# Optimization experiments

Measured on AMD Instinct MI355X. Metric: run time of the kernel, lower is better.

## Reference

```python
import jax, jax.numpy as jnp
import numpy as np

NH, NKV, HD = 16, 4, 128
ROPE_THETA = 10000.0


def setup_inputs() -> dict:
    key = jax.random.key(0)
    ks = jax.random.split(key, 5)
    std = jnp.float32(0.02)
    return {
        "hidden_states": jax.random.normal(ks[0], (1, 2048, 2048), jnp.float32),
        "wq": jax.random.normal(ks[1], (2048, NH * HD), jnp.float32) * std,
        "wk": jax.random.normal(ks[2], (2048, NKV * HD), jnp.float32) * std,
        "wv": jax.random.normal(ks[3], (2048, NKV * HD), jnp.float32) * std,
        "wo": jax.random.normal(ks[4], (NH * HD, 2048), jnp.float32) * std,
    }


def _rope(x, cos, sin):
    # x: [B,S,n,hd]; pairs (even,odd) treated as complex, multiplied by cis(angle)
    xr = x.reshape(*x.shape[:-1], HD // 2, 2)
    re, im = xr[..., 0], xr[..., 1]
    c = cos[None, :, None, :]  # [1,S,1,hd/2]
    s = sin[None, :, None, :]
    out = jnp.stack((re * c - im * s, re * s + im * c), axis=-1)
    return out.reshape(x.shape)


def reference(hidden_states, wq, wk, wv, wo):
    B, S, H = hidden_states.shape
    q = (hidden_states @ wq).reshape(B, S, NH, HD)
    k = (hidden_states @ wk).reshape(B, S, NKV, HD)
    v = (hidden_states @ wv).reshape(B, S, NKV, HD)

    # precompute_freqs_cis (full rotary dim, rot_dim=None)
    freqs = 1.0 / (ROPE_THETA ** (jnp.arange(0, HD, 2, dtype=jnp.float32) / HD))
    ang = jnp.outer(jnp.arange(S, dtype=jnp.float32), freqs)  # [S, hd/2]
    cos, sin = jnp.cos(ang), jnp.sin(ang)

    q = _rope(q.astype(jnp.float32), cos, sin)
    k = _rope(k.astype(jnp.float32), cos, sin)

    # GQA: repeat_kv == repeat_interleave over head axis
    n_rep = NH // NKV
    k = jnp.repeat(k, n_rep, axis=2)  # [B,S,NH,HD]
    v = jnp.repeat(v, n_rep, axis=2)

    scale = jnp.float32(1.0 / np.sqrt(HD))
    scores = jnp.einsum("bqhd,bkhd->bhqk", q, k) * scale
    causal = jnp.tril(jnp.ones((S, S), dtype=bool))
    scores = jnp.where(causal[None, None], scores, jnp.float32(-1e9))
    attn = jax.nn.softmax(scores, axis=-1)
    out = jnp.einsum("bhqk,bkhd->bqhd", attn, v).reshape(B, S, NH * HD)
    return out @ wo
```

## Files before the change

### kernel.cpp

```cpp
#include <hip/hip_runtime.h>
#include <cstdint>

typedef __attribute__((ext_vector_type(8))) short short8;
typedef __attribute__((ext_vector_type(4))) float f32x4;

static __device__ __forceinline__ unsigned short f2bf(float x) {
  union { float f; unsigned int u; } c; c.f = x;
  unsigned int u = c.u;
  unsigned int r = (u + 0x7fffu + ((u >> 16) & 1u)) >> 16;
  return (unsigned short)r;
}

static __device__ __forceinline__ float bf2f(unsigned short x) {
  union { unsigned int u; float f; } c; c.u = ((unsigned int)x) << 16;
  return c.f;
}

static __device__ __forceinline__ void gl_lds16(const void* g, void* l) {
  __builtin_amdgcn_global_load_lds((const __attribute__((address_space(1))) void*)g,
                                   (__attribute__((address_space(3))) void*)l, 16, 0, 0);
}

__global__ __launch_bounds__(256) void k_sincos(float2* __restrict__ ctab) {
  int idx = blockIdx.x * 256 + threadIdx.x;
  int s = idx >> 6, i = idx & 63;
  float freq = powf(10000.0f, -(float)i / 64.0f);
  float sn, cs;
  sincosf((float)s * freq, &sn, &cs);
  ctab[idx] = make_float2(cs, sn);
}

__global__ __launch_bounds__(256) void k_f32_to_bf16(const float* __restrict__ src,
                                                     unsigned short* __restrict__ dst,
                                                     int n4) {
  int i = blockIdx.x * 256 + threadIdx.x;
  if (i >= n4) return;
  float4 v = reinterpret_cast<const float4*>(src)[i];
  ushort4 o;
  o.x = f2bf(v.x); o.y = f2bf(v.y); o.z = f2bf(v.z); o.w = f2bf(v.w);
  reinterpret_cast<ushort4*>(dst)[i] = o;
}

__global__ __launch_bounds__(256) void k_transpose_all(const float* __restrict__ wq,
                                                       const float* __restrict__ wk,
                                                       const float* __restrict__ wv,
                                                       const float* __restrict__ wo,
                                                       unsigned short* __restrict__ wqt,
                                                       unsigned short* __restrict__ wkt,
                                                       unsigned short* __restrict__ wvt,
                                                       unsigned short* __restrict__ wot) {
  __shared__ float tile[32][33];
  int id = blockIdx.x;
  const float* src; unsigned short* dst; int N, t;
  if (id < 4096)       { src = wq; dst = wqt; N = 2048; t = id; }
  else if (id < 8192)  { src = wo; dst = wot; N = 2048; t = id - 4096; }
  else if (id < 9216)  { src = wk; dst = wkt; N = 512;  t = id - 8192; }
  else                 { src = wv; dst = wvt; N = 512;  t = id - 9216; }
  const int K = 2048;
  int ntx = N >> 5;
  int bn = (t % ntx) * 32, bk = (t / ntx) * 32;
  int tx = threadIdx.x & 31, ty = threadIdx.x >> 5;
#pragma unroll
  for (int i = 0; i < 32; i += 8)
    tile[ty + i][tx] = src[(size_t)(bk + ty + i) * N + bn + tx];
  __syncthreads();
#pragma unroll
  for (int i = 0; i < 32; i += 8)
    dst[(size_t)(bn + ty + i) * K + bk + tx] = f2bf(tile[tx][ty + i]);
}

__global__ __launch_bounds__(256) void k_gemm_bf16(const unsigned short* __restrict__ A,
                                                   const unsigned short* __restrict__ Bt,
                                                   float* __restrict__ C,
                                                   unsigned short* __restrict__ Qd,
                                                   unsigned short* __restrict__ Kd,
                                                   unsigned short* __restrict__ VT,
                                                   const float2* __restrict__ ctab,
                                                   int M, int N, int K, int fuse) {
  __shared__ short sA[2][128 * 64];
  __shared__ short sB[2][64 * 64];
  int tid = threadIdx.x;
  int lane = tid & 63, wid = tid >> 6;
  int wr = wid >> 1, wc = wid & 1;

  int gx = gridDim.x, nwg = gx * gridDim.y;
  int flat = blockIdx.y * gx + blockIdx.x;
  int l = (flat & 7) * (nwg >> 3) + (flat >> 3);
  int bx = l % gx, by = l / gx;
  int m0 = by * 128, n0 = bx * 64;

  f32x4 acc[4][2] = {};

  int srcCol = (((tid & 7) ^ ((tid >> 3) & 7)) << 3);
  int rA = tid >> 3;
  const unsigned short* Ag = A + (size_t)(m0 + rA) * K + srcCol;
  const unsigned short* Bg = Bt + (size_t)(n0 + rA) * K + srcCol;
  int wb = (tid & ~63) * 8;

  int g = lane >> 4, fr = lane & 15, sw = fr & 7;

#define STAGE_G(buf, kof) do { \
    gl_lds16(Ag + (kof),                    &sA[buf][wb]); \
    gl_lds16(Ag + 32 * (size_t)K + (kof),   &sA[buf][2048 + wb]); \
    gl_lds16(Ag + 64 * (size_t)K + (kof),   &sA[buf][4096 + wb]); \
    gl_lds16(Ag + 96 * (size_t)K + (kof),   &sA[buf][6144 + wb]); \
    gl_lds16(Bg + (kof),                    &sB[buf][wb]); \
    gl_lds16(Bg + 32 * (size_t)K + (kof),   &sB[buf][2048 + wb]); \
  } while (0)

  int nt = K >> 6;
  STAGE_G(0, 0);
  __syncthreads();

  int cur = 0;
  for (int t = 0; t < nt; t++) {
    if (t + 1 < nt) STAGE_G(cur ^ 1, (size_t)((t + 1) << 6));
    const short* sAc = sA[cur];
    const short* sBc = sB[cur];
#pragma unroll
    for (int kk = 0; kk < 2; kk++) {
      int so = ((((kk << 2) + g) ^ sw) << 3);
      short8 af[4], bf2[2];
#pragma unroll
      for (int x = 0; x < 4; x++)
        af[x] = *(const short8*)(sAc + (wr * 64 + x * 16 + fr) * 64 + so);
#pragma unroll
      for (int ni = 0; ni < 2; ni++)
        bf2[ni] = *(const short8*)(sBc + (wc * 32 + ni * 16 + fr) * 64 + so);
#pragma unroll
      for (int x = 0; x < 4; x++)
#pragma unroll
        for (int ni = 0; ni < 2; ni++)
          acc[x][ni] = __builtin_amdgcn_mfma_f32_16x16x32_bf16(af[x], bf2[ni], acc[x][ni], 0, 0, 0);
    }
    __syncthreads();
    cur ^= 1;
  }
#undef STAGE_G

  int rb = m0 + wr * 64 + (g << 2);
  if (!fuse) {
#pragma unroll
    for (int ni = 0; ni < 2; ni++) {
      int col = n0 + wc * 32 + ni * 16 + fr;
#pragma unroll
      for (int x = 0; x < 4; x++)
#pragma unroll
        for (int j = 0; j < 4; j++)
          C[(size_t)(rb + x * 16 + j) * N + col] = acc[x][ni][j];
    }
    return;
  }

  const float QAMP = 0.12751742836257666f;
#pragma unroll
  for (int ni = 0; ni < 2; ni++) {
    int col = n0 + wc * 32 + ni * 16 + fr;
    if (col >= 2560) {
#pragma unroll
      for (int x = 0; x < 4; x++) {
        ushort4 pk;
        pk.x = f2bf(acc[x][ni][0]); pk.y = f2bf(acc[x][ni][1]);
        pk.z = f2bf(acc[x][ni][2]); pk.w = f2bf(acc[x][ni][3]);
        *(ushort4*)(VT + (size_t)(col - 2560) * 2048 + rb + x * 16) = pk;
      }
    } else {
      int ipair = (col & 127) >> 1;
      bool even = (col & 1) == 0;
      bool isQ = col < 2048;
      unsigned short* dst = isQ ? Qd : Kd;
      int stride = isQ ? 2048 : 512;
      int dcol = isQ ? col : (col - 2048);
      float amp = isQ ? QAMP : 1.0f;
#pragma unroll
      for (int x = 0; x < 4; x++) {
        f32x4 a = acc[x][ni];
        float p0 = __shfl_xor(a[0], 1), p1 = __shfl_xor(a[1], 1);
        float p2 = __shfl_xor(a[2], 1), p3 = __shfl_xor(a[3], 1);
        float pv[4] = {p0, p1, p2, p3};
#pragma unroll
        for (int j = 0; j < 4; j++) {
          int r = rb + x * 16 + j;
          float2 cs = ctab[r * 64 + ipair];
          float o = even ? (a[j] * cs.x - pv[j] * cs.y)
                         : (pv[j] * cs.y + a[j] * cs.x);
          dst[(size_t)r * stride + dcol] = f2bf(o * amp);
        }
      }
    }
  }
}

#define KSTR 136
#define VSTR 72
#define PSTR 72
__global__ __launch_bounds__(256) void k_attn_mfma(const unsigned short* __restrict__ Qb,
                                                   const unsigned short* __restrict__ Kb,
                                                   const unsigned short* __restrict__ Vt,
                                                   unsigned short* __restrict__ O,
                                                   unsigned short* __restrict__ pO,
                                                   float* __restrict__ pML) {
  __shared__ short sK[2][64 * KSTR];
  __shared__ short sV[2][128 * VSTR];
  __shared__ short sP[4][16 * PSTR];
  int h = blockIdx.y;
  int k3 = blockIdx.x / 3, r3 = blockIdx.x % 3;
  int item = (r3 == 0) ? (15 - k3) : ((r3 == 1) ? (47 - 2 * k3) : (46 - 2 * k3));
  int qb, ks, ke, half, mode;
  if (item < 16) {
    qb = item; ks = 0; ke = qb + 1; half = 0; mode = 0;
  } else {
    int i2 = item - 16;
    qb = 16 + (i2 >> 1);
    half = i2 & 1;
    int nh = (qb + 1) >> 1;
    ks = half ? nh : 0;
    ke = half ? (qb + 1) : nh;
    mode = 1;
  }
  int q0 = qb * 64;
  int kvh = h >> 2;
  int tid = threadIdx.x, lane = tid & 63, w = tid >> 6;
  int fr = lane & 15, g = lane >> 4, kq = g << 3;

  short8 qf[4];
  {
    const unsigned short* qrow = Qb + (size_t)(q0 + w * 16 + fr) * 2048 + h * 128 + kq;
#pragma unroll
    for (int ko = 0; ko < 4; ko++) qf[ko] = *(const short8*)(qrow + ko * 32);
  }

  f32x4 oacc[8];
#pragma unroll
  for (int nd = 0; nd < 8; nd++) oacc[nd] = (f32x4){0.f, 0.f, 0.f, 0.f};
  float m_i = -3e38f;
  float l_i = 0.f;

  int skr = tid >> 2, skc = (tid & 3) << 5;
  int svd = tid >> 1, svc = (tid & 1) << 5;
  const unsigned short* Kbase = Kb + (size_t)kvh * 128 + skc;
  const unsigned short* Vbase = Vt + (size_t)(kvh * 128 + svd) * 2048 + svc;
  short* pw = (short*)sP[w];
  int kdOff = skr * KSTR + skc;
  int vdOff = svd * VSTR + svc;

  short8 kreg[4], vreg[4];
  {
    const short8* ksrc = (const short8*)(Kbase + (size_t)(ks * 64 + skr) * 512);
    const short8* vsrc = (const short8*)(Vbase + ks * 64);
#pragma unroll
    for (int j = 0; j < 4; j++) { kreg[j] = ksrc[j]; vreg[j] = vsrc[j]; }
  }
  {
    short* kd = sK[0] + kdOff; short* vd = sV[0] + vdOff;
#pragma unroll
    for (int j = 0; j < 4; j++) { *(short8*)(kd + j * 8) = kreg[j]; *(short8*)(vd + j * 8) = vreg[j]; }
  }
  if (ke - ks >= 2) {
    const short8* ksrc = (const short8*)(Kbase + (size_t)((ks + 1) * 64 + skr) * 512);
    const short8* vsrc = (const short8*)(Vbase + (ks + 1) * 64);
#pragma unroll
    for (int j = 0; j < 4; j++) { kreg[j] = ksrc[j]; vreg[j] = vsrc[j]; }
  }
  __syncthreads();

  int qrowS = q0 + w * 16 + fr;

  for (int kt = ks; kt < ke; kt++) {
    int c = (kt - ks) & 1;
    const short* sKc = sK[c];
    const short* sVc = sV[c];

    f32x4 sacc[4];
#pragma unroll
    for (int ni = 0; ni < 4; ni++) sacc[ni] = (f32x4){0.f, 0.f, 0.f, 0.f};
    __builtin_amdgcn_s_setprio(1);
#pragma unroll
    for (int ko = 0; ko < 4; ko++)
#pragma unroll
      for (int ni = 0; ni < 4; ni++) {
        short8 kf = *(const short8*)(sKc + (ni * 16 + fr) * KSTR + kq + ko * 32);
        sacc[ni] = __builtin_amdgcn_mfma_f32_16x16x32_bf16(kf, qf[ko], sacc[ni], 0, 0, 0);
      }
    __builtin_amdgcn_s_setprio(0);

    if (kt == qb) {
      int k0 = kt * 64;
#pragma unroll
      for (int ni = 0; ni < 4; ni++) {
        int kc = k0 + ni * 16 + (g << 2);
#pragma unroll
        for (int j = 0; j < 4; j++)
          if (kc + j > qrowS) sacc[ni][j] = -3e38f;
      }
    }

    float tm = sacc[0][0];
#pragma unroll
    for (int ni = 0; ni < 4; ni++)
#pragma unroll
      for (int j = 0; j < 4; j++) tm = fmaxf(tm, sacc[ni][j]);
    tm = fmaxf(tm, __shfl_xor(tm, 16));
    tm = fmaxf(tm, __shfl_xor(tm, 32));

    if (!__all(tm <= m_i + 8.0f)) {
      float mn = fmaxf(m_i, tm);
      float sc = exp2f(m_i - mn);
      m_i = mn;
      float scj[4];
#pragma unroll
      for (int j = 0; j < 4; j++) scj[j] = __shfl(sc, (g << 2) + j);
#pragma unroll
      for (int nd = 0; nd < 8; nd++)
#pragma unroll
        for (int j = 0; j < 4; j++) oacc[nd][j] *= scj[j];
      l_i *= sc;
    }

    float ps = 0.f;
#pragma unroll
    for (int ni = 0; ni < 4; ni++) {
      float p0 = exp2f(sacc[ni][0] - m_i);
      float p1 = exp2f(sacc[ni][1] - m_i);
      float p2 = exp2f(sacc[ni][2] - m_i);
      float p3 = exp2f(sacc[ni][3] - m_i);
      ps += (p0 + p1) + (p2 + p3);
      ushort4 pk;
      pk.x = f2bf(p0); pk.y = f2bf(p1); pk.z = f2bf(p2); pk.w = f2bf(p3);
      *(ushort4*)(pw + fr * PSTR + ni * 16 + (g << 2)) = pk;
    }
    ps += __shfl_xor(ps, 16);
    ps += __shfl_xor(ps, 32);
    l_i += ps;

    __builtin_amdgcn_s_setprio(1);
#pragma unroll
    for (int ksl = 0; ksl < 2; ksl++) {
      short8 pa = *(const short8*)(pw + fr * PSTR + kq + ksl * 32);
#pragma unroll
      for (int nd = 0; nd < 8; nd++) {
        short8 vb = *(const short8*)(sVc + (nd * 16 + fr) * VSTR + kq + ksl * 32);
        oacc[nd] = __builtin_amdgcn_mfma_f32_16x16x32_bf16(pa, vb, oacc[nd], 0, 0, 0);
      }
    }
    __builtin_amdgcn_s_setprio(0);

    if (kt + 1 < ke) {
      short* kd = sK[c ^ 1] + kdOff; short* vd = sV[c ^ 1] + vdOff;
#pragma unroll
      for (int j = 0; j < 4; j++) { *(short8*)(kd + j * 8) = kreg[j]; *(short8*)(vd + j * 8) = vreg[j]; }
      if (kt + 2 < ke) {
        int k2 = (kt + 2) * 64;
        const short8* ksrc = (const short8*)(Kbase + (size_t)(k2 + skr) * 512);
        const short8* vsrc = (const short8*)(Vbase + k2);
#pragma unroll
        for (int j = 0; j < 4; j++) { kreg[j] = ksrc[j]; vreg[j] = vsrc[j]; }
      }
      __syncthreads();
    }
  }

  if (mode == 0) {
    int orow = q0 + w * 16 + (g << 2);
#pragma unroll
    for (int j = 0; j < 4; j++) {
      float lj = __shfl(l_i, (g << 2) + j);
      float inv = 1.0f / lj;
#pragma unroll
      for (int nd = 0; nd < 8; nd++)
        O[(size_t)(orow + j) * 2048 + h * 128 + nd * 16 + fr] = f2bf(oacc[nd][j] * inv);
    }
  } else {
    size_t base = ((size_t)(h * 16 + (qb - 16)) * 2 + half) * 64;
    int rl0 = w * 16 + (g << 2);
#pragma unroll
    for (int j = 0; j < 4; j++)
#pragma unroll
      for (int nd = 0; nd < 8; nd++)
        pO[(base + rl0 + j) * 128 + nd * 16 + fr] = f2bf(oacc[nd][j]);
    if (g == 0) {
      size_t r = base + w * 16 + fr;
      pML[r * 2] = m_i;
      pML[r * 2 + 1] = l_i;
    }
  }
}

__global__ __launch_bounds__(256) void k_combine(const unsigned short* __restrict__ pO,
                                                 const float* __restrict__ pML,
                                                 unsigned short* __restrict__ O) {
  int t = blockIdx.x * 256 + threadIdx.x;
  int col = t & 127;
  int rg = t >> 7;
  int h = rg >> 10, rl = rg & 1023;
  size_t r0 = ((size_t)(h * 16 + (rl >> 6)) * 2 + 0) * 64 + (rl & 63);
  size_t r1 = ((size_t)(h * 16 + (rl >> 6)) * 2 + 1) * 64 + (rl & 63);
  float m0 = pML[r0 * 2], l0 = pML[r0 * 2 + 1];
  float m1 = pML[r1 * 2], l1 = pML[r1 * 2 + 1];
  float M = fmaxf(m0, m1);
  float w0 = exp2f(m0 - M), w1 = exp2f(m1 - M);
  float inv = 1.0f / (w0 * l0 + w1 * l1);
  float o0 = bf2f(pO[r0 * 128 + col]);
  float o1 = bf2f(pO[r1 * 128 + col]);
  O[(size_t)(1024 + rl) * 2048 + h * 128 + col] = f2bf((w0 * o0 + w1 * o1) * inv);
}

extern "C" void kernel_launch(void* const* d_in, const int* in_sizes, int n_in,
                              void* d_out, int out_size, void* d_ws, size_t ws_size,
                              hipStream_t stream) {
  const float* hs = (const float*)d_in[0];
  const float* wq = (const float*)d_in[1];
  const float* wk = (const float*)d_in[2];
  const float* wv = (const float*)d_in[3];
  const float* wo = (const float*)d_in[4];
  char* ws = (char*)d_ws;

  unsigned short* hb   = (unsigned short*)(ws);
  unsigned short* wqt  = (unsigned short*)(ws + 8388608);
  unsigned short* wkt  = (unsigned short*)(ws + 16777216);
  unsigned short* wvt  = (unsigned short*)(ws + 18874368);
  unsigned short* wot  = (unsigned short*)(ws + 20971520);
  unsigned short* q_bf = (unsigned short*)(ws + 29360128);
  unsigned short* k_bf = (unsigned short*)(ws + 37748736);
  unsigned short* vt_bf= (unsigned short*)(ws + 39845888);
  float2* ctab         = (float2*)(ws + 41943040);
  unsigned short* ao   = hb;
  unsigned short* pO   = wqt;
  float* pML           = (float*)wkt;
  float* out = (float*)d_out;

  k_sincos<<<512, 256, 0, stream>>>(ctab);
  k_f32_to_bf16<<<4096, 256, 0, stream>>>(hs, hb, 2048 * 2048 / 4);
  k_transpose_all<<<10240, 256, 0, stream>>>(wq, wk, wv, wo, wqt, wkt, wvt, wot);

  k_gemm_bf16<<<dim3(48, 16), 256, 0, stream>>>(hb, wqt, (float*)nullptr,
                                                q_bf, k_bf, vt_bf, ctab,
                                                2048, 3072, 2048, 1);

  k_attn_mfma<<<dim3(48, 16), 256, 0, stream>>>(q_bf, k_bf, vt_bf, ao, pO, pML);
  k_combine<<<8192, 256, 0, stream>>>(pO, pML, ao);

  k_gemm_bf16<<<dim3(32, 16), 256, 0, stream>>>(ao, wot, out,
                                                (unsigned short*)nullptr,
                                                (unsigned short*)nullptr,
                                                (unsigned short*)nullptr,
                                                (const float2*)nullptr,
                                                2048, 2048, 2048, 0);
}
```

Measured before the change: 156.5 us.

## Merge prep kernels, single-buffer attention LDS, packed bf16 convert, reorder work

The three preprocessing kernels (sincos table, hidden-state bf16 conversion, weight transposes) are merged into one launch, which removes two kernel launches. The attention kernel drops its double-buffered K/V shared memory in favor of a single buffer with an extra barrier before each refill. This lowers LDS use and may allow more blocks per CU, but it serializes the LDS store behind compute. The kernel also replaces the per-element bf16 rounding with the packed v_cvt_pk_bf16_f32 instruction, uses a tree max reduction, and schedules the split long query blocks first.

```diff
diff --git a/kernel.cpp b/kernel.cpp
--- a/kernel.cpp
+++ b/kernel.cpp
@@ -16,41 +16,47 @@
   return c.f;
 }
 
+static __device__ __forceinline__ unsigned int cvt_pk_bf16(float a, float b) {
+  unsigned int r;
+  asm("v_cvt_pk_bf16_f32 %0, %1, %2" : "=v"(r) : "v"(a), "v"(b));
+  return r;
+}
+
 static __device__ __forceinline__ void gl_lds16(const void* g, void* l) {
   __builtin_amdgcn_global_load_lds((const __attribute__((address_space(1))) void*)g,
                                    (__attribute__((address_space(3))) void*)l, 16, 0, 0);
 }
 
-__global__ __launch_bounds__(256) void k_sincos(float2* __restrict__ ctab) {
-  int idx = blockIdx.x * 256 + threadIdx.x;
-  int s = idx >> 6, i = idx & 63;
-  float freq = powf(10000.0f, -(float)i / 64.0f);
-  float sn, cs;
-  sincosf((float)s * freq, &sn, &cs);
-  ctab[idx] = make_float2(cs, sn);
-}
-
-__global__ __launch_bounds__(256) void k_f32_to_bf16(const float* __restrict__ src,
-                                                     unsigned short* __restrict__ dst,
-                                                     int n4) {
-  int i = blockIdx.x * 256 + threadIdx.x;
-  if (i >= n4) return;
-  float4 v = reinterpret_cast<const float4*>(src)[i];
-  ushort4 o;
-  o.x = f2bf(v.x); o.y = f2bf(v.y); o.z = f2bf(v.z); o.w = f2bf(v.w);
-  reinterpret_cast<ushort4*>(dst)[i] = o;
-}
-
-__global__ __launch_bounds__(256) void k_transpose_all(const float* __restrict__ wq,
-                                                       const float* __restrict__ wk,
-                                                       const float* __restrict__ wv,
-                                                       const float* __restrict__ wo,
-                                                       unsigned short* __restrict__ wqt,
-                                                       unsigned short* __restrict__ wkt,
-                                                       unsigned short* __restrict__ wvt,
-                                                       unsigned short* __restrict__ wot) {
+__global__ __launch_bounds__(256) void k_prep(const float* __restrict__ wq,
+                                              const float* __restrict__ wk,
+                                              const float* __restrict__ wv,
+                                              const float* __restrict__ wo,
+                                              const float* __restrict__ hs,
+                                              unsigned short* __restrict__ wqt,
+                                              unsigned short* __restrict__ wkt,
+                                              unsigned short* __restrict__ wvt,
+                                              unsigned short* __restrict__ wot,
+                                              unsigned short* __restrict__ hb,
+                                              float2* __restrict__ ctab) {
+  int id = blockIdx.x;
+  if (id >= 10240) {
+    if (id < 14336) {
+      int i = (id - 10240) * 256 + threadIdx.x;
+      float4 v = reinterpret_cast<const float4*>(hs)[i];
+      ushort4 o;
+      o.x = f2bf(v.x); o.y = f2bf(v.y); o.z = f2bf(v.z); o.w = f2bf(v.w);
+      reinterpret_cast<ushort4*>(hb)[i] = o;
+    } else {
+      int idx = (id - 14336) * 256 + threadIdx.x;
+      int s = idx >> 6, i = idx & 63;
+      float freq = powf(10000.0f, -(float)i / 64.0f);
+      float sn, cs;
+      sincosf((float)s * freq, &sn, &cs);
+      ctab[idx] = make_float2(cs, sn);
+    }
+    return;
+  }
   __shared__ float tile[32][33];
-  int id = blockIdx.x;
   const float* src; unsigned short* dst; int N, t;
   if (id < 4096)       { src = wq; dst = wqt; N = 2048; t = id; }
   else if (id < 8192)  { src = wo; dst = wot; N = 2048; t = id - 4096; }
@@ -200,23 +206,21 @@
                                                    unsigned short* __restrict__ O,
                                                    unsigned short* __restrict__ pO,
                                                    float* __restrict__ pML) {
-  __shared__ short sK[2][64 * KSTR];
-  __shared__ short sV[2][128 * VSTR];
+  __shared__ short sK[64 * KSTR];
+  __shared__ short sV[128 * VSTR];
   __shared__ short sP[4][16 * PSTR];
   int h = blockIdx.y;
-  int k3 = blockIdx.x / 3, r3 = blockIdx.x % 3;
-  int item = (r3 == 0) ? (15 - k3) : ((r3 == 1) ? (47 - 2 * k3) : (46 - 2 * k3));
+  int x = blockIdx.x;
   int qb, ks, ke, half, mode;
-  if (item < 16) {
-    qb = item; ks = 0; ke = qb + 1; half = 0; mode = 0;
-  } else {
-    int i2 = item - 16;
-    qb = 16 + (i2 >> 1);
-    half = i2 & 1;
+  if (x < 32) {
+    qb = 31 - (x >> 1);
+    half = x & 1;
     int nh = (qb + 1) >> 1;
     ks = half ? nh : 0;
     ke = half ? (qb + 1) : nh;
     mode = 1;
+  } else {
+    qb = 47 - x; ks = 0; ke = qb + 1; half = 0; mode = 0;
   }
   int q0 = qb * 64;
   int kvh = h >> 2;
@@ -241,8 +245,8 @@
   const unsigned short* Kbase = Kb + (size_t)kvh * 128 + skc;
   const unsigned short* Vbase = Vt + (size_t)(kvh * 128 + svd) * 2048 + svc;
   short* pw = (short*)sP[w];
-  int kdOff = skr * KSTR + skc;
-  int vdOff = svd * VSTR + svc;
+  short* kdst = sK + skr * KSTR + skc;
+  short* vdst = sV + svd * VSTR + svc;
 
   short8 kreg[4], vreg[4];
   {
@@ -251,12 +255,9 @@
 #pragma unroll
     for (int j = 0; j < 4; j++) { kreg[j] = ksrc[j]; vreg[j] = vsrc[j]; }
   }
-  {
-    short* kd = sK[0] + kdOff; short* vd = sV[0] + vdOff;
-#pragma unroll
-    for (int j = 0; j < 4; j++) { *(short8*)(kd + j * 8) = kreg[j]; *(short8*)(vd + j * 8) = vreg[j]; }
-  }
-  if (ke - ks >= 2) {
+#pragma unroll
+  for (int j = 0; j < 4; j++) { *(short8*)(kdst + j * 8) = kreg[j]; *(short8*)(vdst + j * 8) = vreg[j]; }
+  if (ks + 1 < ke) {
     const short8* ksrc = (const short8*)(Kbase + (size_t)((ks + 1) * 64 + skr) * 512);
     const short8* vsrc = (const short8*)(Vbase + (ks + 1) * 64);
 #pragma unroll
@@ -267,10 +268,6 @@
   int qrowS = q0 + w * 16 + fr;
 
   for (int kt = ks; kt < ke; kt++) {
-    int c = (kt - ks) & 1;
-    const short* sKc = sK[c];
-    const short* sVc = sV[c];
-
     f32x4 sacc[4];
 #pragma unroll
     for (int ni = 0; ni < 4; ni++) sacc[ni] = (f32x4){0.f, 0.f, 0.f, 0.f};
@@ -279,7 +276,7 @@
     for (int ko = 0; ko < 4; ko++)
 #pragma unroll
       for (int ni = 0; ni < 4; ni++) {
-        short8 kf = *(const short8*)(sKc + (ni * 16 + fr) * KSTR + kq + ko * 32);
+        short8 kf = *(const short8*)(sK + (ni * 16 + fr) * KSTR + kq + ko * 32);
         sacc[ni] = __builtin_amdgcn_mfma_f32_16x16x32_bf16(kf, qf[ko], sacc[ni], 0, 0, 0);
       }
     __builtin_amdgcn_s_setprio(0);
@@ -295,11 +292,11 @@
       }
     }
 
-    float tm = sacc[0][0];
-#pragma unroll
-    for (int ni = 0; ni < 4; ni++)
-#pragma unroll
-      for (int j = 0; j < 4; j++) tm = fmaxf(tm, sacc[ni][j]);
+    float t0m = fmaxf(fmaxf(sacc[0][0], sacc[0][1]), fmaxf(sacc[0][2], sacc[0][3]));
+    float t1m = fmaxf(fmaxf(sacc[1][0], sacc[1][1]), fmaxf(sacc[1][2], sacc[1][3]));
+    float t2m = fmaxf(fmaxf(sacc[2][0], sacc[2][1]), fmaxf(sacc[2][2], sacc[2][3]));
+    float t3m = fmaxf(fmaxf(sacc[3][0], sacc[3][1]), fmaxf(sacc[3][2], sacc[3][3]));
+    float tm = fmaxf(fmaxf(t0m, t1m), fmaxf(t2m, t3m));
     tm = fmaxf(tm, __shfl_xor(tm, 16));
     tm = fmaxf(tm, __shfl_xor(tm, 32));
 
@@ -325,9 +322,10 @@
       float p2 = exp2f(sacc[ni][2] - m_i);
       float p3 = exp2f(sacc[ni][3] - m_i);
       ps += (p0 + p1) + (p2 + p3);
-      ushort4 pk;
-      pk.x = f2bf(p0); pk.y = f2bf(p1); pk.z = f2bf(p2); pk.w = f2bf(p3);
-      *(ushort4*)(pw + fr * PSTR + ni * 16 + (g << 2)) = pk;
+      uint2 pk;
+      pk.x = cvt_pk_bf16(p0, p1);
+      pk.y = cvt_pk_bf16(p2, p3);
+      *(uint2*)(pw + fr * PSTR + ni * 16 + (g << 2)) = pk;
     }
     ps += __shfl_xor(ps, 16);
     ps += __shfl_xor(ps, 32);
@@ -339,16 +337,16 @@
       short8 pa = *(const short8*)(pw + fr * PSTR + kq + ksl * 32);
 #pragma unroll
       for (int nd = 0; nd < 8; nd++) {
-        short8 vb = *(const short8*)(sVc + (nd * 16 + fr) * VSTR + kq + ksl * 32);
+        short8 vb = *(const short8*)(sV + (nd * 16 + fr) * VSTR + kq + ksl * 32);
         oacc[nd] = __builtin_amdgcn_mfma_f32_16x16x32_bf16(pa, vb, oacc[nd], 0, 0, 0);
       }
     }
     __builtin_amdgcn_s_setprio(0);
 
     if (kt + 1 < ke) {
-      short* kd = sK[c ^ 1] + kdOff; short* vd = sV[c ^ 1] + vdOff;
-#pragma unroll
-      for (int j = 0; j < 4; j++) { *(short8*)(kd + j * 8) = kreg[j]; *(short8*)(vd + j * 8) = vreg[j]; }
+      __syncthreads();
+#pragma unroll
+      for (int j = 0; j < 4; j++) { *(short8*)(kdst + j * 8) = kreg[j]; *(short8*)(vdst + j * 8) = vreg[j]; }
       if (kt + 2 < ke) {
         int k2 = (kt + 2) * 64;
         const short8* ksrc = (const short8*)(Kbase + (size_t)(k2 + skr) * 512);
@@ -429,9 +427,7 @@
   float* pML           = (float*)wkt;
   float* out = (float*)d_out;
 
-  k_sincos<<<512, 256, 0, stream>>>(ctab);
-  k_f32_to_bf16<<<4096, 256, 0, stream>>>(hs, hb, 2048 * 2048 / 4);
-  k_transpose_all<<<10240, 256, 0, stream>>>(wq, wk, wv, wo, wqt, wkt, wvt, wot);
+  k_prep<<<14848, 256, 0, stream>>>(wq, wk, wv, wo, hs, wqt, wkt, wvt, wot, hb, ctab);
 
   k_gemm_bf16<<<dim3(48, 16), 256, 0, stream>>>(hb, wqt, (float*)nullptr,
                                                 q_bf, k_bf, vt_bf, ctab,
```

Result: no change. 156.5 us (+0.0%).
